# Kernel tuning notes

Measured on AMD Instinct MI355X. Metric: run time of the kernel, lower is better.

The kernel has to match this reference:

```python
import jax, jax.numpy as jnp
import numpy as np

B, T, F = 2048, 2048, 12   # n_locations, seq_len, input features
E, P, H = 4, 4, 4          # embedding_dim, pre_hidden, n_hidden
D1, D3, OUT = 4, 6, 1      # hidden dense sizes, output_dim


def setup_inputs() -> dict:
    key = jax.random.key(0)
    ks = jax.random.split(key, 14)
    s = lambda k, shape, fan_in: jax.random.normal(k, shape, jnp.float32) / np.sqrt(fan_in)
    return {
        "x": jax.random.normal(ks[0], (B, T, F), jnp.float32),
        "embed": s(ks[1], (B, E), 1.0),            # Embed table, rows = arange(n_locations)
        "W1": s(ks[2], (F + E, D1), F + E), "b1": jnp.zeros((D1,), jnp.float32),
        "W2": s(ks[3], (D1, P), D1),        "b2": jnp.zeros((P,), jnp.float32),
        "Wi": s(ks[4], (P, H), P),          "bi": jnp.zeros((H,), jnp.float32),
        "Wh": s(ks[5], (H, H), H),          # SimpleCell h2h has no bias in flax
        "W3": s(ks[6], (H, D3), H),         "b3": jnp.zeros((D3,), jnp.float32),
        "W4": s(ks[7], (D3, OUT), D3),      "b4": jnp.zeros((OUT,), jnp.float32),
    }


def reference(x, embed, W1, b1, W2, b2, Wi, bi, Wh, W3, b3, W4, b4):
    # loc = Embed(arange(n_locations)) -> the full table; broadcast over time.
    Tn = x.shape[1]
    loc = jnp.broadcast_to(embed[:, None, :], (embed.shape[0], Tn, embed.shape[1]))
    h = jnp.concatenate([x, loc], axis=-1)            # [B, T, F+E]
    h = jax.nn.relu(h @ W1 + b1)                      # Dense(4) + relu (dropout: no-op, deterministic)
    h = h @ W2 + b2                                   # Dense(pre_hidden)
    # SimpleCell: h_t = tanh(Dense_i(x_t) + Dense_h(h_{t-1})); precompute input proj.
    xi = h @ Wi + bi                                  # [B, T, H]
    h0 = jnp.zeros((x.shape[0], Wh.shape[0]), x.dtype)

    def step(carry, xt):
        new_h = jnp.tanh(xt + carry @ Wh)
        return new_h, new_h

    _, ys = jax.lax.scan(step, h0, jnp.swapaxes(xi, 0, 1))  # scan over time: [T, B, H]
    y = jnp.swapaxes(ys, 0, 1)                        # [B, T, H]
    y = jax.nn.relu(y @ W3 + b3)                      # Dense(6) + relu
    return y @ W4 + b4                                # Dense(output_dim)
```

## Files before the change

### kernel.cpp

```cpp
#include <hip/hip_runtime.h>
#include <hip/hip_fp16.h>


using u32 = unsigned int;
using u16 = unsigned short;

#define B_N 2048
#define T_N 2048

typedef __fp16 f16x2 __attribute__((ext_vector_type(2)));

__device__ __forceinline__ float bfh(u16 v){ return __uint_as_float(((u32)v) << 16); }
__device__ __forceinline__ float lo16(u32 u){ return __uint_as_float(u << 16); }
__device__ __forceinline__ float hi16(u32 u){ return __uint_as_float(u & 0xFFFF0000u); }
__device__ __forceinline__ u16 f2bf(float f){
  u32 u = __float_as_uint(f);
  return (u16)((u + 0x7FFFu + ((u >> 16) & 1u)) >> 16);
}
__device__ __forceinline__ u32 pk2(float a, float b){
  union { f16x2 h; u32 u; } cv;
  cv.h = __builtin_amdgcn_cvt_pkrtz(a, b);
  return cv.u;
}
__device__ __forceinline__ float xlo(u32 w){ return __half2float(__ushort_as_half((u16)(w & 0xFFFFu))); }
__device__ __forceinline__ float xhi(u32 w){ return __half2float(__ushort_as_half((u16)(w >> 16))); }

#define S_PRE 2.8853900817779268f
#define S_NEG (-5.7707801635558537f)

__device__ __forceinline__ bool probe_f32(const void* xraw, int lane){
  const u16* xu = (const u16*)xraw;
  u32 e = (xu[2*lane] >> 7) & 0xFF;
  unsigned long long m = __ballot(e >= 110 && e <= 140);
  return __popcll(m) < 32;
}
__device__ __forceinline__ float ldsel(const void* p, int i, bool f32){
  return f32 ? ((const float*)p)[i] : bfh(((const u16*)p)[i]);
}

__global__ __launch_bounds__(256) void k_xi(const void* __restrict__ xraw,
                                            const void* __restrict__ embed,
                                            const void* __restrict__ W1,
                                            const void* __restrict__ b1,
                                            const void* __restrict__ W2,
                                            const void* __restrict__ b2,
                                            const void* __restrict__ Wi,
                                            const void* __restrict__ bi,
                                            const void* __restrict__ Wh,
                                            u32* __restrict__ xi2)
{
  __shared__ u32 sx[12320];
  __shared__ float sc[104];
  const int tid = threadIdx.x;
  const int b0 = (blockIdx.x >> 4) << 3;
  const int t0 = (blockIdx.x & 15) << 7;

  if (tid < 64) {
    const bool f32 = probe_f32(xraw, tid);
    if (tid == 0) sc[100] = f32 ? 1.0f : 0.0f;
    if (tid < 48) sc[tid] = ldsel(W1, tid, f32);
    else {
      int i = tid - 48, r = i >> 2, c = i & 3;
      float s = 0.f;
      for (int p = 0; p < 4; ++p) s += ldsel(W2, r*4+p, f32) * ldsel(Wi, p*4+c, f32);
      sc[48 + i] = S_PRE * s;
    }
    if (tid < 4) {
      int c = tid;
      float s = ldsel(bi, c, f32);
      for (int p = 0; p < 4; ++p) s += ldsel(b2, p, f32) * ldsel(Wi, p*4+c, f32);
      float sw = 0.f;
      for (int k = 0; k < 4; ++k) sw += ldsel(Wh, k*4+c, f32);
      sc[64 + c] = S_PRE * (s + sw);
    }
    if (tid < 32) {
      int r = tid >> 2, c = tid & 3;
      int b = b0 + r;
      float s = ldsel(b1, c, f32);
      for (int e = 0; e < 4; ++e)
        s += ldsel(embed, b*4+e, f32) * ldsel(W1, (12+e)*4+c, f32);
      sc[68 + tid] = s;
    }
  }
  __syncthreads();
  const bool f32 = sc[100] > 0.5f;

  const int RS  = f32 ? 1540 : 772;
  const int CPT = f32 ? 12 : 6;
  const int K   = f32 ? 12 : 6;

  {
    const int r = tid >> 5, c = tid & 31;
    const size_t rowbase_u32 = ((size_t)(b0 + r) * T_N + t0) * (size_t)CPT;
    const uint4* gsrc = (const uint4*)((const u32*)xraw + rowbase_u32);
    uint4* ldst = (uint4*)(sx + r * RS);
    for (int k = 0; k < K; ++k)
      ldst[c + 32*k] = gsrc[c + 32*k];
  }
  __syncthreads();

  float W1f[48];
#pragma unroll
  for (int i = 0; i < 48; ++i) W1f[i] = sc[i];
  float Wc[16];
#pragma unroll
  for (int i = 0; i < 16; ++i) Wc[i] = sc[48+i];
  float bc[4];
#pragma unroll
  for (int i = 0; i < 4; ++i) bc[i] = sc[64+i];

  const int r = tid & 7, t4l = tid >> 3;
  const int b = b0 + r;
  const int T4 = (t0 >> 2) + t4l;
  float p1[4];
#pragma unroll
  for (int i = 0; i < 4; ++i) p1[i] = sc[68 + r*4 + i];

  float acc[4][4];
#pragma unroll
  for (int ti = 0; ti < 4; ++ti) {
    const u32* sp = sx + r * RS + (t4l*4 + ti) * CPT;
    float xf[12];
    if (f32) {
#pragma unroll
      for (int f = 0; f < 12; ++f) xf[f] = __uint_as_float(sp[f]);
    } else {
#pragma unroll
      for (int w = 0; w < 6; ++w) {
        u32 u = sp[w];
        xf[2*w]   = lo16(u);
        xf[2*w+1] = hi16(u);
      }
    }
    float h1[4];
#pragma unroll
    for (int c = 0; c < 4; ++c) {
      float s = p1[c];
#pragma unroll
      for (int f = 0; f < 12; ++f) s = fmaf(xf[f], W1f[f*4+c], s);
      h1[c] = fmaxf(s, 0.f);
    }
#pragma unroll
    for (int c = 0; c < 4; ++c) {
      float s = bc[c];
#pragma unroll
      for (int k = 0; k < 4; ++k) s = fmaf(h1[k], Wc[k*4+c], s);
      acc[c][ti] = s;
    }
  }
  u32 w[8];
#pragma unroll
  for (int j = 0; j < 4; ++j) {
    w[j*2]   = pk2(acc[j][0], acc[j][1]);
    w[j*2+1] = pk2(acc[j][2], acc[j][3]);
  }
  u32* dst = xi2 + ((size_t)T4 * B_N + b) * 8;
  *(uint4*)(dst)     = make_uint4(w[0], w[1], w[2], w[3]);
  *(uint4*)(dst + 4) = make_uint4(w[4], w[5], w[6], w[7]);
}

template<int CTRL>
__device__ __forceinline__ float dppf(float v) {
  return __int_as_float(__builtin_amdgcn_mov_dpp(__float_as_int(v), CTRL, 0xF, 0xF, true));
}

__global__ __launch_bounds__(64) void k_scan(const void* __restrict__ xraw,
                                             const void* __restrict__ Wh,
                                             const u32* __restrict__ xi2,
                                             u32* __restrict__ hbuf)
{
  const int tid = threadIdx.x;
  const bool f32 = probe_f32(xraw, tid);

  const int g = blockIdx.x * 64 + tid;
  const int b = g >> 2, j = g & 3;
  const float u0 = S_NEG * ldsel(Wh, (j<<2) + j, f32);
  const float u1 = S_NEG * ldsel(Wh, ((j^1)<<2) + j, f32);
  const float u2 = S_NEG * ldsel(Wh, ((j^2)<<2) + j, f32);
  const float u3 = S_NEG * ldsel(Wh, ((j^3)<<2) + j, f32);

  const uint2* xp = (const uint2*)xi2 + (size_t)b*4 + j;
  uint2* hp = (uint2*)hbuf + (size_t)b * (T_N/4) * 4 + j;

  constexpr int D = 8;
  uint2 buf[D];
#pragma unroll
  for (int i = 0; i < D; ++i) buf[i] = xp[(size_t)i * (B_N*4)];

  float r = 0.5f;
  for (int tb = 0; tb < T_N/4; tb += D) {
#pragma unroll
    for (int q = 0; q < D; ++q) {
      uint2 xiv = buf[q];
      int pf = tb + q + D; pf = pf < (T_N/4 - 1) ? pf : (T_N/4 - 1);
      buf[q] = xp[(size_t)pf * (B_N*4)];
      float bases[4] = {xlo(xiv.x), xhi(xiv.x), xlo(xiv.y), xhi(xiv.y)};
      float hv[4];
#pragma unroll
      for (int ti = 0; ti < 4; ++ti) {
        float rs  = r;
        float rx1 = dppf<0xB1>(rs);
        float rx2 = dppf<0x4E>(rs);
        float rx3 = dppf<0x1B>(rs);
        float pa = fmaf(u0, rs,  bases[ti]);
        float pb = fmaf(u1, rx1, pa);
        float pc = u2 * rx2;
        float pd = fmaf(u3, rx3, pc);
        float z  = pb + pd;
        float e  = __builtin_amdgcn_exp2f(z);
        r = __builtin_amdgcn_rcpf(e + 1.0f);
        hv[ti] = fmaf(-2.0f, r, 1.0f);
      }
      hp[(size_t)(tb + q) * 4] = make_uint2(pk2(hv[0], hv[1]), pk2(hv[2], hv[3]));
    }
  }
}

__global__ __launch_bounds__(256) void k_out(const void* __restrict__ xraw,
                                             const void* __restrict__ W3,
                                             const void* __restrict__ b3,
                                             const void* __restrict__ W4,
                                             const void* __restrict__ b4,
                                             const u32* __restrict__ hbuf,
                                             void* __restrict__ outp)
{
  __shared__ float sc[40];
  const int tid = threadIdx.x;
  if (tid < 64) {
    const bool f32 = probe_f32(xraw, tid);
    if (tid == 0) sc[37] = f32 ? 1.0f : 0.0f;
    if (tid < 24)                sc[tid]      = ldsel(W3, tid, f32);
    else if (tid < 30)           sc[tid]      = ldsel(b3, tid - 24, f32);
    else if (tid < 36)           sc[tid]      = ldsel(W4, tid - 30, f32);
    else if (tid == 36)          sc[36]       = ldsel(b4, 0, f32);
  }
  __syncthreads();
  const bool f32 = sc[37] > 0.5f;

  float W3f[24], b3f[6], W4f[6];
#pragma unroll
  for (int i = 0; i < 24; ++i) W3f[i] = sc[i];
#pragma unroll
  for (int i = 0; i < 6; ++i)  b3f[i] = sc[24+i];
#pragma unroll
  for (int i = 0; i < 6; ++i)  W4f[i] = sc[30+i];
  const float b4f = sc[36];

  const int g = blockIdx.x * 256 + tid;
  const int b = g >> 9;
  const int t4 = g & 511;

  const uint4* hp = (const uint4*)hbuf + (size_t)(b * 512 + t4) * 2;
  uint4 q0 = hp[0], q1 = hp[1];
  u32 wj[4][2] = {{q0.x,q0.y},{q0.z,q0.w},{q1.x,q1.y},{q1.z,q1.w}};

  float res[4];
#pragma unroll
  for (int s = 0; s < 4; ++s) {
    float h0 = (s&1) ? xhi(wj[0][s>>1]) : xlo(wj[0][s>>1]);
    float h1 = (s&1) ? xhi(wj[1][s>>1]) : xlo(wj[1][s>>1]);
    float h2 = (s&1) ? xhi(wj[2][s>>1]) : xlo(wj[2][s>>1]);
    float h3 = (s&1) ? xhi(wj[3][s>>1]) : xlo(wj[3][s>>1]);
    float a = b4f;
#pragma unroll
    for (int m = 0; m < 6; ++m) {
      float y = b3f[m];
      y = fmaf(h0, W3f[0*6+m], y);
      y = fmaf(h1, W3f[1*6+m], y);
      y = fmaf(h2, W3f[2*6+m], y);
      y = fmaf(h3, W3f[3*6+m], y);
      y = fmaxf(y, 0.f);
      a = fmaf(y, W4f[m], a);
    }
    res[s] = a;
  }
  if (f32) {
    *((float4*)outp + ((size_t)b * 512 + t4)) = make_float4(res[0], res[1], res[2], res[3]);
  } else {
    uint2 pk;
    pk.x = (u32)f2bf(res[0]) | ((u32)f2bf(res[1]) << 16);
    pk.y = (u32)f2bf(res[2]) | ((u32)f2bf(res[3]) << 16);
    *((uint2*)outp + ((size_t)b * 512 + t4)) = pk;
  }
}

extern "C" void kernel_launch(void* const* d_in, const int* in_sizes, int n_in,
                              void* d_out, int out_size, void* d_ws, size_t ws_size,
                              hipStream_t stream)
{
  u32* xi2  = (u32*)d_ws;
  u32* hbuf = (u32*)((char*)d_ws + (size_t)B_N*T_N*4*2);

  k_xi  <<<4096, 256, 0, stream>>>(d_in[0], d_in[1], d_in[2], d_in[3], d_in[4],
                                   d_in[5], d_in[6], d_in[7], d_in[8], xi2);
  k_scan<<<128, 64, 0, stream>>>(d_in[0], d_in[8], xi2, hbuf);
  k_out <<<4096, 256, 0, stream>>>(d_in[0], d_in[9], d_in[10], d_in[11], d_in[12],
                                   hbuf, d_out);
}
```

Measured before the change: 389.3 us.

## Fuse output head into scan kernel via producer/consumer waves and LDS ring

```diff
diff --git a/kernel.cpp b/kernel.cpp
--- a/kernel.cpp
+++ b/kernel.cpp
@@ -164,123 +164,123 @@
   return __int_as_float(__builtin_amdgcn_mov_dpp(__float_as_int(v), CTRL, 0xF, 0xF, true));
 }
 
-__global__ __launch_bounds__(64) void k_scan(const void* __restrict__ xraw,
-                                             const void* __restrict__ Wh,
-                                             const u32* __restrict__ xi2,
-                                             u32* __restrict__ hbuf)
+__device__ __forceinline__ float sel_h(uint2 v, int sel){
+  u32 w = (sel & 2) ? v.y : v.x;
+  w >>= ((sel & 1) << 4);
+  return __half2float(__ushort_as_half((u16)(w & 0xFFFFu)));
+}
+
+__global__ __launch_bounds__(128) void k_scan(const void* __restrict__ xraw,
+                                              const void* __restrict__ Wh,
+                                              const u32* __restrict__ xi2,
+                                              const void* __restrict__ W3,
+                                              const void* __restrict__ b3,
+                                              const void* __restrict__ W4,
+                                              const void* __restrict__ b4,
+                                              void* __restrict__ outp)
 {
+  __shared__ uint2 sring[8][64];
+  __shared__ u32 scnt[2];
+  volatile u32* vwr = &scnt[0];
+  volatile u32* vrd = &scnt[1];
+
   const int tid = threadIdx.x;
-  const bool f32 = probe_f32(xraw, tid);
-
-  const int g = blockIdx.x * 64 + tid;
-  const int b = g >> 2, j = g & 3;
-  const float u0 = S_NEG * ldsel(Wh, (j<<2) + j, f32);
-  const float u1 = S_NEG * ldsel(Wh, ((j^1)<<2) + j, f32);
-  const float u2 = S_NEG * ldsel(Wh, ((j^2)<<2) + j, f32);
-  const float u3 = S_NEG * ldsel(Wh, ((j^3)<<2) + j, f32);
-
-  const uint2* xp = (const uint2*)xi2 + (size_t)b*4 + j;
-  uint2* hp = (uint2*)hbuf + (size_t)b * (T_N/4) * 4 + j;
-
-  constexpr int D = 8;
-  uint2 buf[D];
-#pragma unroll
-  for (int i = 0; i < D; ++i) buf[i] = xp[(size_t)i * (B_N*4)];
-
-  float r = 0.5f;
-  for (int tb = 0; tb < T_N/4; tb += D) {
-#pragma unroll
-    for (int q = 0; q < D; ++q) {
-      uint2 xiv = buf[q];
-      int pf = tb + q + D; pf = pf < (T_N/4 - 1) ? pf : (T_N/4 - 1);
-      buf[q] = xp[(size_t)pf * (B_N*4)];
-      float bases[4] = {xlo(xiv.x), xhi(xiv.x), xlo(xiv.y), xhi(xiv.y)};
-      float hv[4];
-#pragma unroll
-      for (int ti = 0; ti < 4; ++ti) {
-        float rs  = r;
-        float rx1 = dppf<0xB1>(rs);
-        float rx2 = dppf<0x4E>(rs);
-        float rx3 = dppf<0x1B>(rs);
-        float pa = fmaf(u0, rs,  bases[ti]);
-        float pb = fmaf(u1, rx1, pa);
-        float pc = u2 * rx2;
-        float pd = fmaf(u3, rx3, pc);
-        float z  = pb + pd;
-        float e  = __builtin_amdgcn_exp2f(z);
-        r = __builtin_amdgcn_rcpf(e + 1.0f);
-        hv[ti] = fmaf(-2.0f, r, 1.0f);
+  const int lane = tid & 63;
+  if (tid < 2) scnt[tid] = 0;
+  __syncthreads();
+
+  const bool f32 = probe_f32(xraw, lane);
+
+  if (tid < 64) {
+    const int g = blockIdx.x * 64 + lane;
+    const int b = g >> 2, j = g & 3;
+    const float u0 = S_NEG * ldsel(Wh, (j<<2) + j, f32);
+    const float u1 = S_NEG * ldsel(Wh, ((j^1)<<2) + j, f32);
+    const float u2 = S_NEG * ldsel(Wh, ((j^2)<<2) + j, f32);
+    const float u3 = S_NEG * ldsel(Wh, ((j^3)<<2) + j, f32);
+
+    const uint2* xp = (const uint2*)xi2 + (size_t)b*4 + j;
+
+    constexpr int D = 8;
+    uint2 buf[D];
+#pragma unroll
+    for (int i = 0; i < D; ++i) buf[i] = xp[(size_t)i * (B_N*4)];
+
+    float r = 0.5f;
+    u32 rdseen = 0;
+    for (int tb = 0; tb < T_N/4; tb += D) {
+#pragma unroll
+      for (int q = 0; q < D; ++q) {
+        const u32 t4i = (u32)(tb + q);
+        uint2 xiv = buf[q];
+        int pf = tb + q + D; pf = pf < (T_N/4 - 1) ? pf : (T_N/4 - 1);
+        buf[q] = xp[(size_t)pf * (B_N*4)];
+        if (t4i >= 8u) { while (rdseen + 8u <= t4i) rdseen = *vrd; }
+        float bases[4] = {xlo(xiv.x), xhi(xiv.x), xlo(xiv.y), xhi(xiv.y)};
+        float hv[4];
+#pragma unroll
+        for (int ti = 0; ti < 4; ++ti) {
+          float rs  = r;
+          float rx1 = dppf<0xB1>(rs);
+          float rx2 = dppf<0x4E>(rs);
+          float rx3 = dppf<0x1B>(rs);
+          float pa = fmaf(u0, rs,  bases[ti]);
+          float pb = fmaf(u1, rx1, pa);
+          float pc = u2 * rx2;
+          float pd = fmaf(u3, rx3, pc);
+          float z  = pb + pd;
+          float e  = __builtin_amdgcn_exp2f(z);
+          r = __builtin_amdgcn_rcpf(e + 1.0f);
+          hv[ti] = fmaf(-2.0f, r, 1.0f);
+        }
+        sring[t4i & 7u][lane] = make_uint2(pk2(hv[0], hv[1]), pk2(hv[2], hv[3]));
+        __asm__ volatile("" ::: "memory");
+        if (lane == 0) *vwr = t4i + 1u;
       }
-      hp[(size_t)(tb + q) * 4] = make_uint2(pk2(hv[0], hv[1]), pk2(hv[2], hv[3]));
-    }
-  }
-}
-
-__global__ __launch_bounds__(256) void k_out(const void* __restrict__ xraw,
-                                             const void* __restrict__ W3,
-                                             const void* __restrict__ b3,
-                                             const void* __restrict__ W4,
-                                             const void* __restrict__ b4,
-                                             const u32* __restrict__ hbuf,
-                                             void* __restrict__ outp)
-{
-  __shared__ float sc[40];
-  const int tid = threadIdx.x;
-  if (tid < 64) {
-    const bool f32 = probe_f32(xraw, tid);
-    if (tid == 0) sc[37] = f32 ? 1.0f : 0.0f;
-    if (tid < 24)                sc[tid]      = ldsel(W3, tid, f32);
-    else if (tid < 30)           sc[tid]      = ldsel(b3, tid - 24, f32);
-    else if (tid < 36)           sc[tid]      = ldsel(W4, tid - 30, f32);
-    else if (tid == 36)          sc[36]       = ldsel(b4, 0, f32);
-  }
-  __syncthreads();
-  const bool f32 = sc[37] > 0.5f;
-
-  float W3f[24], b3f[6], W4f[6];
-#pragma unroll
-  for (int i = 0; i < 24; ++i) W3f[i] = sc[i];
-#pragma unroll
-  for (int i = 0; i < 6; ++i)  b3f[i] = sc[24+i];
-#pragma unroll
-  for (int i = 0; i < 6; ++i)  W4f[i] = sc[30+i];
-  const float b4f = sc[36];
-
-  const int g = blockIdx.x * 256 + tid;
-  const int b = g >> 9;
-  const int t4 = g & 511;
-
-  const uint4* hp = (const uint4*)hbuf + (size_t)(b * 512 + t4) * 2;
-  uint4 q0 = hp[0], q1 = hp[1];
-  u32 wj[4][2] = {{q0.x,q0.y},{q0.z,q0.w},{q1.x,q1.y},{q1.z,q1.w}};
-
-  float res[4];
-#pragma unroll
-  for (int s = 0; s < 4; ++s) {
-    float h0 = (s&1) ? xhi(wj[0][s>>1]) : xlo(wj[0][s>>1]);
-    float h1 = (s&1) ? xhi(wj[1][s>>1]) : xlo(wj[1][s>>1]);
-    float h2 = (s&1) ? xhi(wj[2][s>>1]) : xlo(wj[2][s>>1]);
-    float h3 = (s&1) ? xhi(wj[3][s>>1]) : xlo(wj[3][s>>1]);
-    float a = b4f;
+    }
+  } else {
+    const int s = lane >> 2, tw = lane & 3;
+    const size_t brow = (size_t)(blockIdx.x * 16 + s) * (size_t)T_N;
+    float W3p0[6], W3p1[6], W3p2[6], W3p3[6], b3f[6], W4f[6];
 #pragma unroll
     for (int m = 0; m < 6; ++m) {
-      float y = b3f[m];
-      y = fmaf(h0, W3f[0*6+m], y);
-      y = fmaf(h1, W3f[1*6+m], y);
-      y = fmaf(h2, W3f[2*6+m], y);
-      y = fmaf(h3, W3f[3*6+m], y);
-      y = fmaxf(y, 0.f);
-      a = fmaf(y, W4f[m], a);
-    }
-    res[s] = a;
-  }
-  if (f32) {
-    *((float4*)outp + ((size_t)b * 512 + t4)) = make_float4(res[0], res[1], res[2], res[3]);
-  } else {
-    uint2 pk;
-    pk.x = (u32)f2bf(res[0]) | ((u32)f2bf(res[1]) << 16);
-    pk.y = (u32)f2bf(res[2]) | ((u32)f2bf(res[3]) << 16);
-    *((uint2*)outp + ((size_t)b * 512 + t4)) = pk;
+      W3p0[m] = ldsel(W3, (tw    )*6 + m, f32);
+      W3p1[m] = ldsel(W3, (tw ^ 1)*6 + m, f32);
+      W3p2[m] = ldsel(W3, (tw ^ 2)*6 + m, f32);
+      W3p3[m] = ldsel(W3, (tw ^ 3)*6 + m, f32);
+      b3f[m]  = ldsel(b3, m, f32);
+      W4f[m]  = ldsel(W4, m, f32);
+    }
+    const float b4f = ldsel(b4, 0, f32);
+
+    u32 wrseen = 0;
+    for (u32 t4i = 0; t4i < T_N/4; ++t4i) {
+      if (wrseen <= t4i) { do { wrseen = *vwr; } while (wrseen <= t4i); }
+      __asm__ volatile("" ::: "memory");
+      uint2 v = sring[t4i & 7u][lane];
+      __asm__ volatile("" ::: "memory");
+      if (lane == 0) *vrd = t4i + 1u;
+
+      float h0 = sel_h(v, tw);
+      float h1 = dppf<0xB1>(sel_h(v, tw ^ 1));
+      float h2 = dppf<0x4E>(sel_h(v, tw ^ 2));
+      float h3 = dppf<0x1B>(sel_h(v, tw ^ 3));
+
+      float a = b4f;
+#pragma unroll
+      for (int m = 0; m < 6; ++m) {
+        float y = b3f[m];
+        y = fmaf(h0, W3p0[m], y);
+        y = fmaf(h1, W3p1[m], y);
+        y = fmaf(h2, W3p2[m], y);
+        y = fmaf(h3, W3p3[m], y);
+        y = fmaxf(y, 0.f);
+        a = fmaf(y, W4f[m], a);
+      }
+      const size_t t = brow + (size_t)t4i*4 + (size_t)tw;
+      if (f32) ((float*)outp)[t] = a;
+      else     ((u16*)outp)[t]   = f2bf(a);
+    }
   }
 }
 
@@ -288,12 +288,10 @@
                               void* d_out, int out_size, void* d_ws, size_t ws_size,
                               hipStream_t stream)
 {
-  u32* xi2  = (u32*)d_ws;
-  u32* hbuf = (u32*)((char*)d_ws + (size_t)B_N*T_N*4*2);
+  u32* xi2 = (u32*)d_ws;
 
   k_xi  <<<4096, 256, 0, stream>>>(d_in[0], d_in[1], d_in[2], d_in[3], d_in[4],
                                    d_in[5], d_in[6], d_in[7], d_in[8], xi2);
-  k_scan<<<128, 64, 0, stream>>>(d_in[0], d_in[8], xi2, hbuf);
-  k_out <<<4096, 256, 0, stream>>>(d_in[0], d_in[9], d_in[10], d_in[11], d_in[12],
-                                   hbuf, d_out);
-}
+  k_scan<<<128, 128, 0, stream>>>(d_in[0], d_in[8], xi2,
+                                  d_in[9], d_in[10], d_in[11], d_in[12], d_out);
+}
```

Result: slower. 469.0 us (+20.5%).

## Store xi batch-major and load x directly from global without LDS staging

Applied to the files above, without the earlier changes.

```diff
diff --git a/kernel.cpp b/kernel.cpp
--- a/kernel.cpp
+++ b/kernel.cpp
@@ -49,15 +49,14 @@
                                             const void* __restrict__ Wh,
                                             u32* __restrict__ xi2)
 {
-  __shared__ u32 sx[12320];
-  __shared__ float sc[104];
+  __shared__ float sc[76];
   const int tid = threadIdx.x;
-  const int b0 = (blockIdx.x >> 4) << 3;
-  const int t0 = (blockIdx.x & 15) << 7;
+  const int b   = blockIdx.x >> 1;
+  const int t4  = ((blockIdx.x & 1) << 8) | tid;
 
   if (tid < 64) {
     const bool f32 = probe_f32(xraw, tid);
-    if (tid == 0) sc[100] = f32 ? 1.0f : 0.0f;
+    if (tid == 0) sc[72] = f32 ? 1.0f : 0.0f;
     if (tid < 48) sc[tid] = ldsel(W1, tid, f32);
     else {
       int i = tid - 48, r = i >> 2, c = i & 3;
@@ -73,31 +72,16 @@
       for (int k = 0; k < 4; ++k) sw += ldsel(Wh, k*4+c, f32);
       sc[64 + c] = S_PRE * (s + sw);
     }
-    if (tid < 32) {
-      int r = tid >> 2, c = tid & 3;
-      int b = b0 + r;
+    if (tid < 4) {
+      int c = tid;
       float s = ldsel(b1, c, f32);
       for (int e = 0; e < 4; ++e)
         s += ldsel(embed, b*4+e, f32) * ldsel(W1, (12+e)*4+c, f32);
-      sc[68 + tid] = s;
+      sc[68 + c] = s;
     }
   }
   __syncthreads();
-  const bool f32 = sc[100] > 0.5f;
-
-  const int RS  = f32 ? 1540 : 772;
-  const int CPT = f32 ? 12 : 6;
-  const int K   = f32 ? 12 : 6;
-
-  {
-    const int r = tid >> 5, c = tid & 31;
-    const size_t rowbase_u32 = ((size_t)(b0 + r) * T_N + t0) * (size_t)CPT;
-    const uint4* gsrc = (const uint4*)((const u32*)xraw + rowbase_u32);
-    uint4* ldst = (uint4*)(sx + r * RS);
-    for (int k = 0; k < K; ++k)
-      ldst[c + 32*k] = gsrc[c + 32*k];
-  }
-  __syncthreads();
+  const bool f32 = sc[72] > 0.5f;
 
   float W1f[48];
 #pragma unroll
@@ -108,36 +92,47 @@
   float bc[4];
 #pragma unroll
   for (int i = 0; i < 4; ++i) bc[i] = sc[64+i];
-
-  const int r = tid & 7, t4l = tid >> 3;
-  const int b = b0 + r;
-  const int T4 = (t0 >> 2) + t4l;
   float p1[4];
 #pragma unroll
-  for (int i = 0; i < 4; ++i) p1[i] = sc[68 + r*4 + i];
+  for (int i = 0; i < 4; ++i) p1[i] = sc[68+i];
+
+  float xf[48];
+  if (f32) {
+    const uint4* gp = (const uint4*)xraw + ((size_t)b * T_N + (size_t)t4*4) * 3;
+    uint4 v[12];
+#pragma unroll
+    for (int k = 0; k < 12; ++k) v[k] = gp[k];
+#pragma unroll
+    for (int k = 0; k < 12; ++k) {
+      xf[k*4+0] = __uint_as_float(v[k].x);
+      xf[k*4+1] = __uint_as_float(v[k].y);
+      xf[k*4+2] = __uint_as_float(v[k].z);
+      xf[k*4+3] = __uint_as_float(v[k].w);
+    }
+  } else {
+    const uint4* gp = (const uint4*)((const u16*)xraw + ((size_t)b * T_N + (size_t)t4*4) * 12);
+    uint4 v[6];
+#pragma unroll
+    for (int k = 0; k < 6; ++k) v[k] = gp[k];
+#pragma unroll
+    for (int k = 0; k < 6; ++k) {
+      xf[k*8+0] = lo16(v[k].x); xf[k*8+1] = hi16(v[k].x);
+      xf[k*8+2] = lo16(v[k].y); xf[k*8+3] = hi16(v[k].y);
+      xf[k*8+4] = lo16(v[k].z); xf[k*8+5] = hi16(v[k].z);
+      xf[k*8+6] = lo16(v[k].w); xf[k*8+7] = hi16(v[k].w);
+    }
+  }
 
   float acc[4][4];
 #pragma unroll
   for (int ti = 0; ti < 4; ++ti) {
-    const u32* sp = sx + r * RS + (t4l*4 + ti) * CPT;
-    float xf[12];
-    if (f32) {
-#pragma unroll
-      for (int f = 0; f < 12; ++f) xf[f] = __uint_as_float(sp[f]);
-    } else {
-#pragma unroll
-      for (int w = 0; w < 6; ++w) {
-        u32 u = sp[w];
-        xf[2*w]   = lo16(u);
-        xf[2*w+1] = hi16(u);
-      }
-    }
+    const float* xt = &xf[ti * 12];
     float h1[4];
 #pragma unroll
     for (int c = 0; c < 4; ++c) {
       float s = p1[c];
 #pragma unroll
-      for (int f = 0; f < 12; ++f) s = fmaf(xf[f], W1f[f*4+c], s);
+      for (int f = 0; f < 12; ++f) s = fmaf(xt[f], W1f[f*4+c], s);
       h1[c] = fmaxf(s, 0.f);
     }
 #pragma unroll
@@ -154,7 +149,7 @@
     w[j*2]   = pk2(acc[j][0], acc[j][1]);
     w[j*2+1] = pk2(acc[j][2], acc[j][3]);
   }
-  u32* dst = xi2 + ((size_t)T4 * B_N + b) * 8;
+  u32* dst = xi2 + ((size_t)b * (T_N/4) + t4) * 8;
   *(uint4*)(dst)     = make_uint4(w[0], w[1], w[2], w[3]);
   *(uint4*)(dst + 4) = make_uint4(w[4], w[5], w[6], w[7]);
 }
@@ -179,13 +174,13 @@
   const float u2 = S_NEG * ldsel(Wh, ((j^2)<<2) + j, f32);
   const float u3 = S_NEG * ldsel(Wh, ((j^3)<<2) + j, f32);
 
-  const uint2* xp = (const uint2*)xi2 + (size_t)b*4 + j;
+  const uint2* xp = (const uint2*)xi2 + (size_t)b * (T_N/4) * 4 + j;
   uint2* hp = (uint2*)hbuf + (size_t)b * (T_N/4) * 4 + j;
 
   constexpr int D = 8;
   uint2 buf[D];
 #pragma unroll
-  for (int i = 0; i < D; ++i) buf[i] = xp[(size_t)i * (B_N*4)];
+  for (int i = 0; i < D; ++i) buf[i] = xp[(size_t)i * 4];
 
   float r = 0.5f;
   for (int tb = 0; tb < T_N/4; tb += D) {
@@ -193,7 +188,7 @@
     for (int q = 0; q < D; ++q) {
       uint2 xiv = buf[q];
       int pf = tb + q + D; pf = pf < (T_N/4 - 1) ? pf : (T_N/4 - 1);
-      buf[q] = xp[(size_t)pf * (B_N*4)];
+      buf[q] = xp[(size_t)pf * 4];
       float bases[4] = {xlo(xiv.x), xhi(xiv.x), xlo(xiv.y), xhi(xiv.y)};
       float hv[4];
 #pragma unroll
@@ -289,7 +284,7 @@
                               hipStream_t stream)
 {
   u32* xi2  = (u32*)d_ws;
-  u32* hbuf = (u32*)((char*)d_ws + (size_t)B_N*T_N*4*2);
+  u32* hbuf = (u32*)((char*)d_ws + (size_t)B_N*(T_N/4)*32);
 
   k_xi  <<<4096, 256, 0, stream>>>(d_in[0], d_in[1], d_in[2], d_in[3], d_in[4],
                                    d_in[5], d_in[6], d_in[7], d_in[8], xi2);
```

New measurement: 379.5 us. -2.5%, faster.
